# Optimization experiments

Hardware: AMD Instinct MI355X
Metric: run time of the kernel (lower is better)

The kernel has to match this reference:

```python
import jax, jax.numpy as jnp
import numpy as np

HIDDEN = 1024
HEADS = 16
HEAD_DIM = HIDDEN // HEADS
SCALE = HEAD_DIM ** -0.5


def setup_inputs() -> dict:
    key = jax.random.key(0)
    ks = jax.random.split(key, 7)
    B, N, T = 4, 64, 128
    x = jax.random.normal(ks[0], (B * N, T, HIDDEN), dtype=jnp.float32)
    bvecs = jax.random.normal(ks[1], (B, T, 3), dtype=jnp.float32)
    w_std = HIDDEN ** -0.5
    qkv_w = jax.random.normal(ks[2], (HIDDEN, 3 * HIDDEN), dtype=jnp.float32) * w_std
    qkv_b = jnp.zeros((3 * HIDDEN,), dtype=jnp.float32)
    proj_w = jax.random.normal(ks[3], (HIDDEN, HIDDEN), dtype=jnp.float32) * w_std
    proj_b = jnp.zeros((HIDDEN,), dtype=jnp.float32)
    angular_bias_scale = jnp.ones((1,), dtype=jnp.float32)
    return {"x": x, "bvecs": bvecs, "qkv_w": qkv_w, "qkv_b": qkv_b,
            "proj_w": proj_w, "proj_b": proj_b,
            "angular_bias_scale": angular_bias_scale}


def reference(x, bvecs, qkv_w, qkv_b, proj_w, proj_b, angular_bias_scale):
    BN, T, D = x.shape
    B = bvecs.shape[0]
    N = BN // B
    # QKV projection -> (3, BN, H, T, hd)
    qkv = (x @ qkv_w + qkv_b).reshape(BN, T, 3, HEADS, HEAD_DIM)
    qkv = jnp.transpose(qkv, (2, 0, 3, 1, 4))
    q, k, v = qkv[0], qkv[1], qkv[2]
    # normalize b-vectors and compute per-batch angular cosine similarity (B, T, T)
    bvecs_n = bvecs / (jnp.linalg.norm(bvecs, axis=-1, keepdims=True) + 1e-6)
    cos_sim = jnp.clip(jnp.einsum('bid,bjd->bij', bvecs_n, bvecs_n), -1.0, 1.0)
    # repeat across the N patches per batch -> (BN, 1, T, T)
    angular_bias = jnp.repeat(cos_sim, N, axis=0)[:, None, :, :]
    attn_logits = jnp.einsum('bhid,bhjd->bhij', q, k) * SCALE
    attn = jax.nn.softmax(attn_logits + angular_bias_scale * angular_bias, axis=-1)
    out = jnp.einsum('bhij,bhjd->bhid', attn, v)
    out = jnp.transpose(out, (0, 2, 1, 3)).reshape(BN, T, D)
    return out @ proj_w + proj_b
```

## Files before the change

### kernel.cpp

```cpp
#include <hip/hip_runtime.h>
#include <hip/hip_bf16.h>
#include <stdint.h>


typedef float f32x4 __attribute__((ext_vector_type(4)));
typedef __bf16 bf16x8 __attribute__((ext_vector_type(8)));
typedef unsigned short us8 __attribute__((ext_vector_type(8)));
typedef unsigned short u16;

#define MROWS 32768

static __device__ __forceinline__ u16 bfbits(float f) {
  __bf16 h = (__bf16)f;
  return __builtin_bit_cast(u16, h);
}
static __device__ __forceinline__ float bff(u16 u) {
  return (float)__builtin_bit_cast(__bf16, u);
}
static __device__ __forceinline__ void gld16(const void* g, void* l) {
  __builtin_amdgcn_global_load_lds(
      (const __attribute__((address_space(1))) void*)g,
      (__attribute__((address_space(3))) void*)l, 16, 0, 0);
}
static __device__ __forceinline__ f32x4 mfma16(bf16x8 a, bf16x8 b, f32x4 c) {
  return __builtin_amdgcn_mfma_f32_16x16x32_bf16(a, b, c, 0, 0, 0);
}

__global__ __launch_bounds__(256) void k_split(const float* __restrict__ x,
                                               u16* __restrict__ xhl, int n4) {
  int i = blockIdx.x * 256 + threadIdx.x;
  if (i >= n4) return;
  float4 v = ((const float4*)x)[i];
  ushort4 h, l;
  h.x = bfbits(v.x); l.x = bfbits(v.x - bff(h.x));
  h.y = bfbits(v.y); l.y = bfbits(v.y - bff(h.y));
  h.z = bfbits(v.z); l.z = bfbits(v.z - bff(h.z));
  h.w = bfbits(v.w); l.w = bfbits(v.w - bff(h.w));
  int i4 = i << 2;
  int r = i4 >> 10, k = i4 & 1023;
  size_t o = ((size_t)r << 11) + (size_t)((k >> 5) << 6) + (k & 31);
  *(ushort4*)(xhl + o) = h;
  *(ushort4*)(xhl + o + 32) = l;
}

__global__ void k_tsplit(const float* __restrict__ w, u16* __restrict__ thl,
                         int K, int N, int remap) {
  __shared__ float tile[32][33];
  int n0 = blockIdx.x * 32, k0 = blockIdx.y * 32;
  int tx = threadIdx.x, ty = threadIdx.y;
#pragma unroll
  for (int j = 0; j < 32; j += 8)
    tile[ty + j][tx] = w[(size_t)(k0 + ty + j) * N + n0 + tx];
  __syncthreads();
#pragma unroll
  for (int j = 0; j < 32; j += 8) {
    float v = tile[tx][ty + j];
    int n = n0 + ty + j;
    int orow = n;
    if (remap) {
      int s = n >> 10, hid = n & 1023;
      orow = (hid >> 8) * 768 + s * 256 + (hid & 255);
    }
    int k = k0 + tx;
    size_t o = ((size_t)orow << 11) + (size_t)((k >> 5) << 6) + (k & 31);
    u16 hb = bfbits(v);
    thl[o] = hb;
    thl[o + 32] = bfbits(v - bff(hb));
  }
}

__global__ void k_gbias(const float* __restrict__ b, float* __restrict__ gb) {
  int n = blockIdx.x * 256 + threadIdx.x;
  if (n >= 3072) return;
  int s = n >> 10, hid = n & 1023;
  gb[(hid >> 8) * 768 + s * 256 + (hid & 255)] = b[n];
}

__global__ void k_cos(const float* __restrict__ bv, float* __restrict__ cosb) {
  int b = blockIdx.x, t = threadIdx.x;
  __shared__ float nb[128][3];
  float x = bv[(b * 128 + t) * 3 + 0];
  float y = bv[(b * 128 + t) * 3 + 1];
  float z = bv[(b * 128 + t) * 3 + 2];
  float inv = 1.0f / (sqrtf(x * x + y * y + z * z) + 1e-6f);
  nb[t][0] = x * inv; nb[t][1] = y * inv; nb[t][2] = z * inv;
  __syncthreads();
  float xn = nb[t][0], yn = nb[t][1], zn = nb[t][2];
  for (int j = 0; j < 128; j++) {
    float c = xn * nb[j][0] + yn * nb[j][1] + zn * nb[j][2];
    c = fminf(1.0f, fmaxf(-1.0f, c));
    cosb[((size_t)b * 128 + t) * 128 + j] = c;
  }
}

template <int AMODE, int MODE>
__global__ __launch_bounds__(512, 2) void k_gemm(
    const u16* __restrict__ Ahl, const float* __restrict__ Af,
    const u16* __restrict__ Bhl, const float* __restrict__ bias,
    float* __restrict__ C) {
  __shared__ __align__(16) u16 sA[3][128 * 64];
  __shared__ __align__(16) u16 sB[3][256 * 64];
  int tid = threadIdx.x;
  int wave = tid >> 6, lane = tid & 63;
  int fr = lane & 15, fq = lane >> 4;
  int wm = wave >> 2, wn = wave & 3;

  int nT = gridDim.y;
  int h = blockIdx.y * gridDim.x + blockIdx.x;
  int nwg = gridDim.x * gridDim.y;
  int w = (h & 7) * (nwg >> 3) + (h >> 3);
  int rowBase = (w / nT) * 128, colBase = (w % nT) * 256;

  f32x4 acc[4][4];
#pragma unroll
  for (int i = 0; i < 4; i++)
#pragma unroll
    for (int j = 0; j < 4; j++) acc[i][j] = (f32x4){0.f, 0.f, 0.f, 0.f};

  int lr = lane >> 3, ls = (lane & 7) ^ lr;
  const u16* aS = Ahl + (size_t)(rowBase + lr) * 2048 + ls * 8;
  const u16* bS = Bhl + (size_t)(colBase + lr) * 2048 + ls * 8;

  auto stageB = [&](int t, int buf) {
#pragma unroll
    for (int q = 0; q < 4; q++) {
      int R = (q * 8 + wave) * 8;
      gld16(bS + (size_t)R * 2048 + t * 64, &sB[buf][R * 64]);
    }
  };
  auto stageA0 = [&](int t, int buf) {
#pragma unroll
    for (int q = 0; q < 2; q++) {
      int R = (q * 8 + wave) * 8;
      gld16(aS + (size_t)R * 2048 + t * 64, &sA[buf][R * 64]);
    }
  };
  auto stageA1 = [&](int t, int buf) {
    int row = tid >> 2, cs = tid & 3;
    const float* src = Af + (size_t)(rowBase + row) * 1024 + t * 32 + cs * 8;
    float4 v0 = *(const float4*)src;
    float4 v1 = *(const float4*)(src + 4);
    float vv[8] = {v0.x, v0.y, v0.z, v0.w, v1.x, v1.y, v1.z, v1.w};
    us8 hv, lv;
#pragma unroll
    for (int i = 0; i < 8; i++) {
      u16 hb = bfbits(vv[i]);
      hv[i] = hb;
      lv[i] = bfbits(vv[i] - bff(hb));
    }
    int sw = row & 7;
    *(us8*)(&sA[buf][row * 64 + ((cs ^ sw) << 3)]) = hv;
    *(us8*)(&sA[buf][row * 64 + (((cs + 4) ^ sw) << 3)]) = lv;
  };
  auto stage = [&](int t, int buf) {
    stageB(t, buf);
    if constexpr (AMODE == 0) stageA0(t, buf);
    else stageA1(t, buf);
  };

  auto tile = [&](int t, int cur, int nbuf, int vmode) {
    const u16* lA = &sA[cur][0];
    const u16* lB = &sB[cur][0];
    bf16x8 fbh[4], fbl[4];
#pragma unroll
    for (int ni = 0; ni < 4; ni++) {
      int c = wn * 64 + ni * 16 + fr;
      int sw = c & 7;
      fbh[ni] = *(const bf16x8*)(&lB[c * 64 + ((fq ^ sw) << 3)]);
      fbl[ni] = *(const bf16x8*)(&lB[c * 64 + (((fq + 4) ^ sw) << 3)]);
    }
    if (t + 2 < 32) stage(t + 2, nbuf);
#pragma unroll
    for (int mi = 0; mi < 4; mi++) {
      bf16x8 fah, fal;
      int r = wm * 64 + mi * 16 + fr;
      int sw = r & 7;
      fah = *(const bf16x8*)(&lA[r * 64 + ((fq ^ sw) << 3)]);
      fal = *(const bf16x8*)(&lA[r * 64 + (((fq + 4) ^ sw) << 3)]);
#pragma unroll
      for (int ni = 0; ni < 4; ni++) {
        acc[mi][ni] = mfma16(fah, fbh[ni], acc[mi][ni]);
        acc[mi][ni] = mfma16(fah, fbl[ni], acc[mi][ni]);
        acc[mi][ni] = mfma16(fal, fbh[ni], acc[mi][ni]);
      }
    }
    if constexpr (AMODE == 1) {
      if (vmode >= 0)
        asm volatile("s_waitcnt vmcnt(0) lgkmcnt(0)" ::: "memory");
    } else {
      if (vmode == 6)
        asm volatile("s_waitcnt vmcnt(6)" ::: "memory");
      else if (vmode == 0)
        asm volatile("s_waitcnt vmcnt(0)" ::: "memory");
    }
    __builtin_amdgcn_s_barrier();
  };

  stage(0, 0);
  stage(1, 1);
  if constexpr (AMODE == 0) {
    asm volatile("s_waitcnt vmcnt(6)" ::: "memory");
  } else {
    asm volatile("s_waitcnt vmcnt(0) lgkmcnt(0)" ::: "memory");
  }
  __builtin_amdgcn_s_barrier();

#pragma unroll 1
  for (int tb = 0; tb < 30; tb += 3) {
    tile(tb, 0, 2, 6);
    tile(tb + 1, 1, 0, 6);
    tile(tb + 2, 2, 1, 6);
  }
  tile(30, 0, 2, 0);
  tile(31, 1, 0, -1);

  u16* C16 = (u16*)C;
#pragma unroll
  for (int mi = 0; mi < 4; mi++)
#pragma unroll
    for (int ni = 0; ni < 4; ni++)
#pragma unroll
      for (int rr = 0; rr < 4; rr++) {
        int row = rowBase + wm * 64 + mi * 16 + fq * 4 + rr;
        int col = colBase + wn * 64 + ni * 16 + fr;
        float v = acc[mi][ni][rr] + bias[col];
        if constexpr (MODE == 0) {
          int s = col >> 8, hl2 = (col >> 6) & 3, d = col & 63;
          int bn = row >> 7, t = row & 127;
          size_t tb_ = (size_t)(bn * 4 + hl2) * 16384;
          u16 hb = bfbits(v);
          u16 lb = bfbits(v - bff(hb));
          size_t o;
          if (s == 2) {
            o = (size_t)33554432 + tb_ + (size_t)((t >> 6) << 12) + d * 64 +
                ((((t >> 3) & 7) ^ (d & 7)) << 3) + (t & 7);
          } else {
            o = (size_t)s * 16777216 + tb_ + t * 64 +
                (((d >> 3) ^ (t & 7)) << 3) + (d & 7);
          }
          C16[o] = hb;
          C16[o + 8192] = lb;
        } else {
          C[(size_t)row * 1024 + col] = v;
        }
      }
}

__global__ __launch_bounds__(256) void k_attn(
    const u16* __restrict__ Qp, const u16* __restrict__ Kp,
    const u16* __restrict__ Vp, const float* __restrict__ cosb,
    const float* __restrict__ absSp, u16* __restrict__ Ohl, int g) {
  __shared__ __align__(16) u16 sKV[2][2][4096];
  __shared__ __align__(16) float sS[64 * 132];
  u16* sP = (u16*)sS;

  int bx = blockIdx.x;
  int half = bx & 1, hl = (bx >> 1) & 3, bn = bx >> 3, b = bn >> 6;
  int tid = threadIdx.x, wave = tid >> 6, lane = tid & 63;
  int fr = lane & 15, fq = lane >> 4;
  size_t tbase = (size_t)(bn * 4 + hl) * 16384;
  float absS = absSp[0];

  const u16* Qt = Qp + tbase;
  const u16* Kt = Kp + tbase;
  const u16* Vt = Vp + tbase;

  auto stageK = [&](int kt, int buf) {
#pragma unroll
    for (int p2 = 0; p2 < 2; p2++)
#pragma unroll
      for (int q = 0; q < 2; q++) {
        int seg = (q * 4 + wave) * 512;
        gld16(Kt + p2 * 8192 + kt * 4096 + seg + lane * 8, &sKV[buf][p2][seg]);
      }
  };
  auto stageV = [&](int vt, int buf) {
#pragma unroll
    for (int p2 = 0; p2 < 2; p2++)
#pragma unroll
      for (int q = 0; q < 2; q++) {
        int seg = (q * 4 + wave) * 512;
        gld16(Vt + p2 * 8192 + vt * 4096 + seg + lane * 8, &sKV[buf][p2][seg]);
      }
  };

  stageK(0, 0);
  __builtin_amdgcn_sched_barrier(0);
  int rowl = wave * 16 + fr;
  int tq = half * 64 + rowl;
  bf16x8 qh[2], ql[2];
#pragma unroll
  for (int ki = 0; ki < 2; ki++) {
    int sl = ((ki * 4 + fq) ^ (tq & 7)) << 3;
    qh[ki] = *(const bf16x8*)(Qt + tq * 64 + sl);
    ql[ki] = *(const bf16x8*)(Qt + 8192 + tq * 64 + sl);
  }
  __builtin_amdgcn_sched_barrier(0);
  stageK(1, 1);
  __builtin_amdgcn_sched_barrier(0);
  asm volatile("s_waitcnt vmcnt(4)" ::: "memory");
  __builtin_amdgcn_s_barrier();

#pragma unroll
  for (int kt = 0; kt < 2; kt++) {
#pragma unroll
    for (int nt = 0; nt < 4; nt++) {
      f32x4 a = (f32x4){0.f, 0.f, 0.f, 0.f};
      int cl = nt * 16 + fr;
#pragma unroll
      for (int ki = 0; ki < 2; ki++) {
        int sl = ((ki * 4 + fq) ^ (cl & 7)) << 3;
        bf16x8 kh = *(const bf16x8*)(&sKV[kt][0][cl * 64 + sl]);
        bf16x8 kl = *(const bf16x8*)(&sKV[kt][1][cl * 64 + sl]);
        a = mfma16(qh[ki], kh, a);
        a = mfma16(qh[ki], kl, a);
        a = mfma16(ql[ki], kh, a);
      }
#pragma unroll
      for (int rr = 0; rr < 4; rr++) {
        int rl = wave * 16 + fq * 4 + rr;
        int col = kt * 64 + nt * 16 + fr;
        int tg = half * 64 + rl;
        float cv = cosb[((size_t)(b * 128 + tg)) * 128 + col];
        sS[rl * 132 + col] = a[rr] * 0.125f + absS * cv;
      }
    }
    __builtin_amdgcn_s_barrier();
    if (kt == 0) {
      stageV(0, 0);
      __builtin_amdgcn_sched_barrier(0);
      asm volatile("s_waitcnt vmcnt(4)" ::: "memory");
      __builtin_amdgcn_s_barrier();
    }
  }
  stageV(1, 1);
  __builtin_amdgcn_sched_barrier(0);

  for (int r = 0; r < 16; r++) {
    int tl = wave * 16 + r;
    float s0 = sS[tl * 132 + lane], s1 = sS[tl * 132 + 64 + lane];
    float m = fmaxf(s0, s1);
#pragma unroll
    for (int off = 32; off >= 1; off >>= 1) m = fmaxf(m, __shfl_xor(m, off));
    float p0 = __expf(s0 - m), p1 = __expf(s1 - m);
    float sum = p0 + p1;
#pragma unroll
    for (int off = 32; off >= 1; off >>= 1) sum += __shfl_xor(sum, off);
    float inv = 1.0f / sum;
    p0 *= inv; p1 *= inv;
    u16 h0 = bfbits(p0), h1 = bfbits(p1);
    sP[tl * 264 + lane] = h0;
    sP[tl * 264 + 64 + lane] = h1;
    sP[tl * 264 + 128 + lane] = bfbits(p0 - bff(h0));
    sP[tl * 264 + 192 + lane] = bfbits(p1 - bff(h1));
  }

  f32x4 accO[4];
#pragma unroll
  for (int nt = 0; nt < 4; nt++) accO[nt] = (f32x4){0.f, 0.f, 0.f, 0.f};
#pragma unroll
  for (int vt = 0; vt < 2; vt++) {
    if (vt == 0) {
      asm volatile("s_waitcnt vmcnt(4)" ::: "memory");
    } else {
      asm volatile("s_waitcnt vmcnt(0)" ::: "memory");
    }
    __builtin_amdgcn_s_barrier();
    bf16x8 ph[2], pl[2];
#pragma unroll
    for (int ki = 0; ki < 2; ki++) {
      ph[ki] = *(const bf16x8*)(&sP[rowl * 264 + vt * 64 + ki * 32 + fq * 8]);
      pl[ki] = *(const bf16x8*)(&sP[rowl * 264 + 128 + vt * 64 + ki * 32 + fq * 8]);
    }
#pragma unroll
    for (int nt = 0; nt < 4; nt++) {
      int d = nt * 16 + fr;
#pragma unroll
      for (int ki = 0; ki < 2; ki++) {
        int sl = ((ki * 4 + fq) ^ (d & 7)) << 3;
        bf16x8 vh = *(const bf16x8*)(&sKV[vt][0][d * 64 + sl]);
        bf16x8 vl = *(const bf16x8*)(&sKV[vt][1][d * 64 + sl]);
        accO[nt] = mfma16(ph[ki], vh, accO[nt]);
        accO[nt] = mfma16(ph[ki], vl, accO[nt]);
        accO[nt] = mfma16(pl[ki], vh, accO[nt]);
      }
    }
  }

  int hg = g * 4 + hl;
#pragma unroll
  for (int nt = 0; nt < 4; nt++)
#pragma unroll
    for (int rr = 0; rr < 4; rr++) {
      int tl = wave * 16 + fq * 4 + rr;
      int tg = half * 64 + tl;
      int d = nt * 16 + fr;
      float v = accO[nt][rr];
      size_t o = ((size_t)(bn * 128 + tg) << 11) +
                 (size_t)(hg * 2 + (d >> 5)) * 64 + (d & 31);
      u16 hh = bfbits(v);
      Ohl[o] = hh;
      Ohl[o + 32] = bfbits(v - bff(hh));
    }
}

extern "C" void kernel_launch(void* const* d_in, const int* in_sizes, int n_in,
                              void* d_out, int out_size, void* d_ws,
                              size_t ws_size, hipStream_t stream) {
  const float* x = (const float*)d_in[0];
  const float* bv = (const float*)d_in[1];
  const float* qkvw = (const float*)d_in[2];
  const float* qkvb = (const float*)d_in[3];
  const float* projw = (const float*)d_in[4];
  const float* projb = (const float*)d_in[5];
  const float* absS = (const float*)d_in[6];
  float* out = (float*)d_out;

  char* ws = (char*)d_ws;
  size_t off = 0;
  auto alloc = [&](size_t b) {
    char* p = ws + off;
    off += (b + 255) & ~(size_t)255;
    return p;
  };
  u16* wqhl = (u16*)alloc((size_t)3072 * 2048 * 2);
  u16* wphl = (u16*)alloc((size_t)1024 * 2048 * 2);
  float* gbias = (float*)alloc(3072 * 4);
  float* cosb = (float*)alloc((size_t)4 * 128 * 128 * 4);
  u16* Ohl = (u16*)alloc((size_t)MROWS * 2048 * 2);
  u16* xhl = (u16*)alloc((size_t)MROWS * 2048 * 2);
  bool planA = (off <= ws_size);

  u16* O16 = (u16*)d_out;

  k_tsplit<<<dim3(96, 32), dim3(32, 8), 0, stream>>>(qkvw, wqhl, 1024, 3072, 1);
  k_tsplit<<<dim3(32, 32), dim3(32, 8), 0, stream>>>(projw, wphl, 1024, 1024, 0);
  k_gbias<<<dim3(12), dim3(256), 0, stream>>>(qkvb, gbias);
  k_cos<<<dim3(4), dim3(128), 0, stream>>>(bv, cosb);
  if (planA)
    k_split<<<dim3(32768), dim3(256), 0, stream>>>(x, xhl, 8388608);

  for (int g = 0; g < 4; g++) {
    const u16* bw = wqhl + (size_t)g * 768 * 2048;
    if (planA)
      k_gemm<0, 0><<<dim3(256, 3), dim3(512), 0, stream>>>(
          xhl, nullptr, bw, gbias + g * 768, (float*)O16);
    else
      k_gemm<1, 0><<<dim3(256, 3), dim3(512), 0, stream>>>(
          nullptr, x, bw, gbias + g * 768, (float*)O16);
    k_attn<<<dim3(2048), dim3(256), 0, stream>>>(
        O16, O16 + 16777216, O16 + 33554432, cosb, absS, Ohl, g);
  }

  k_gemm<0, 1><<<dim3(256, 4), dim3(512), 0, stream>>>(
      Ohl, nullptr, wphl, projb, out);
}
```

Measured before the change: 1.299 ms.

## Stage GEMM and attention epilogues through LDS for coalesced 16-byte stores

The QKV GEMM epilogue now writes its hi/lo bf16 split outputs into a shared-memory tile, then copies the whole contiguous block to global memory with 16-byte vector stores instead of scattered 2-byte stores. The attention kernel likewise stages its output in LDS before writing coalesced uint4 rows. The attention block index is remapped so blocks are grouped differently across dispatch, and s_setprio raises wave priority around the MFMA loops. This trades extra barriers and LDS traffic for far fewer, wider global writes.

Measured after the change: 1.198 ms. -7.8%, faster.

```diff
diff --git a/kernel.cpp b/kernel.cpp
--- a/kernel.cpp
+++ b/kernel.cpp
@@ -98,8 +98,9 @@
     const u16* __restrict__ Ahl, const float* __restrict__ Af,
     const u16* __restrict__ Bhl, const float* __restrict__ bias,
     float* __restrict__ C) {
-  __shared__ __align__(16) u16 sA[3][128 * 64];
-  __shared__ __align__(16) u16 sB[3][256 * 64];
+  __shared__ __align__(16) u16 smem[73728];
+  u16* sAb = smem;
+  u16* sBb = smem + 24576;
   int tid = threadIdx.x;
   int wave = tid >> 6, lane = tid & 63;
   int fr = lane & 15, fq = lane >> 4;
@@ -125,14 +126,14 @@
 #pragma unroll
     for (int q = 0; q < 4; q++) {
       int R = (q * 8 + wave) * 8;
-      gld16(bS + (size_t)R * 2048 + t * 64, &sB[buf][R * 64]);
+      gld16(bS + (size_t)R * 2048 + t * 64, &sBb[buf * 16384 + R * 64]);
     }
   };
   auto stageA0 = [&](int t, int buf) {
 #pragma unroll
     for (int q = 0; q < 2; q++) {
       int R = (q * 8 + wave) * 8;
-      gld16(aS + (size_t)R * 2048 + t * 64, &sA[buf][R * 64]);
+      gld16(aS + (size_t)R * 2048 + t * 64, &sAb[buf * 8192 + R * 64]);
     }
   };
   auto stageA1 = [&](int t, int buf) {
@@ -149,8 +150,8 @@
       lv[i] = bfbits(vv[i] - bff(hb));
     }
     int sw = row & 7;
-    *(us8*)(&sA[buf][row * 64 + ((cs ^ sw) << 3)]) = hv;
-    *(us8*)(&sA[buf][row * 64 + (((cs + 4) ^ sw) << 3)]) = lv;
+    *(us8*)(&sAb[buf * 8192 + row * 64 + ((cs ^ sw) << 3)]) = hv;
+    *(us8*)(&sAb[buf * 8192 + row * 64 + (((cs + 4) ^ sw) << 3)]) = lv;
   };
   auto stage = [&](int t, int buf) {
     stageB(t, buf);
@@ -159,8 +160,8 @@
   };
 
   auto tile = [&](int t, int cur, int nbuf, int vmode) {
-    const u16* lA = &sA[cur][0];
-    const u16* lB = &sB[cur][0];
+    const u16* lA = &sAb[cur * 8192];
+    const u16* lB = &sBb[cur * 16384];
     bf16x8 fbh[4], fbl[4];
 #pragma unroll
     for (int ni = 0; ni < 4; ni++) {
@@ -214,36 +215,49 @@
   tile(30, 0, 2, 0);
   tile(31, 1, 0, -1);
 
-  u16* C16 = (u16*)C;
-#pragma unroll
-  for (int mi = 0; mi < 4; mi++)
-#pragma unroll
-    for (int ni = 0; ni < 4; ni++)
-#pragma unroll
-      for (int rr = 0; rr < 4; rr++) {
-        int row = rowBase + wm * 64 + mi * 16 + fq * 4 + rr;
-        int col = colBase + wn * 64 + ni * 16 + fr;
-        float v = acc[mi][ni][rr] + bias[col];
-        if constexpr (MODE == 0) {
-          int s = col >> 8, hl2 = (col >> 6) & 3, d = col & 63;
-          int bn = row >> 7, t = row & 127;
-          size_t tb_ = (size_t)(bn * 4 + hl2) * 16384;
+  if constexpr (MODE == 0) {
+    int s = colBase >> 8;
+    int bn = rowBase >> 7;
+#pragma unroll
+    for (int mi = 0; mi < 4; mi++)
+#pragma unroll
+      for (int ni = 0; ni < 4; ni++)
+#pragma unroll
+        for (int rr = 0; rr < 4; rr++) {
+          int t = wm * 64 + mi * 16 + fq * 4 + rr;
+          int c256 = wn * 64 + ni * 16 + fr;
+          int d = c256 & 63;
+          float v = acc[mi][ni][rr] + bias[colBase + c256];
           u16 hb = bfbits(v);
           u16 lb = bfbits(v - bff(hb));
-          size_t o;
-          if (s == 2) {
-            o = (size_t)33554432 + tb_ + (size_t)((t >> 6) << 12) + d * 64 +
-                ((((t >> 3) & 7) ^ (d & 7)) << 3) + (t & 7);
-          } else {
-            o = (size_t)s * 16777216 + tb_ + t * 64 +
-                (((d >> 3) ^ (t & 7)) << 3) + (d & 7);
-          }
-          C16[o] = hb;
-          C16[o + 8192] = lb;
-        } else {
-          C[(size_t)row * 1024 + col] = v;
+          int loff;
+          if (s == 2)
+            loff = wn * 16384 + ((t >> 6) << 12) + d * 64 +
+                   ((((t >> 3) & 7) ^ (d & 7)) << 3) + (t & 7);
+          else
+            loff = wn * 16384 + t * 64 + (((d >> 3) ^ (t & 7)) << 3) + (d & 7);
+          smem[loff] = hb;
+          smem[loff + 8192] = lb;
         }
-      }
+    __syncthreads();
+    u16* C16 = (u16*)C;
+    size_t gbase = (size_t)s * 16777216 + (size_t)bn * 65536;
+    const uint4* srcv = (const uint4*)smem;
+    uint4* dstv = (uint4*)(C16 + gbase);
+#pragma unroll
+    for (int i = 0; i < 16; i++) dstv[i * 512 + tid] = srcv[i * 512 + tid];
+  } else {
+#pragma unroll
+    for (int mi = 0; mi < 4; mi++)
+#pragma unroll
+      for (int ni = 0; ni < 4; ni++)
+#pragma unroll
+        for (int rr = 0; rr < 4; rr++) {
+          int row = rowBase + wm * 64 + mi * 16 + fq * 4 + rr;
+          int col = colBase + wn * 64 + ni * 16 + fr;
+          C[(size_t)row * 1024 + col] = acc[mi][ni][rr] + bias[col];
+        }
+  }
 }
 
 __global__ __launch_bounds__(256) void k_attn(
@@ -253,9 +267,12 @@
   __shared__ __align__(16) u16 sKV[2][2][4096];
   __shared__ __align__(16) float sS[64 * 132];
   u16* sP = (u16*)sS;
-
-  int bx = blockIdx.x;
-  int half = bx & 1, hl = (bx >> 1) & 3, bn = bx >> 3, b = bn >> 6;
+  u16* sO = (u16*)sS;
+
+  int v_ = blockIdx.x;
+  int pair = (v_ & 7) * 128 + ((v_ >> 3) >> 1);
+  int half = (v_ >> 3) & 1;
+  int hl = pair & 3, bn = pair >> 2, b = bn >> 6;
   int tid = threadIdx.x, wave = tid >> 6, lane = tid & 63;
   int fr = lane & 15, fq = lane >> 4;
   size_t tbase = (size_t)(bn * 4 + hl) * 16384;
@@ -303,6 +320,7 @@
 
 #pragma unroll
   for (int kt = 0; kt < 2; kt++) {
+    __builtin_amdgcn_s_setprio(1);
 #pragma unroll
     for (int nt = 0; nt < 4; nt++) {
       f32x4 a = (f32x4){0.f, 0.f, 0.f, 0.f};
@@ -325,6 +343,7 @@
         sS[rl * 132 + col] = a[rr] * 0.125f + absS * cv;
       }
     }
+    __builtin_amdgcn_s_setprio(0);
     __builtin_amdgcn_s_barrier();
     if (kt == 0) {
       stageV(0, 0);
@@ -372,6 +391,7 @@
       ph[ki] = *(const bf16x8*)(&sP[rowl * 264 + vt * 64 + ki * 32 + fq * 8]);
       pl[ki] = *(const bf16x8*)(&sP[rowl * 264 + 128 + vt * 64 + ki * 32 + fq * 8]);
     }
+    __builtin_amdgcn_s_setprio(1);
 #pragma unroll
     for (int nt = 0; nt < 4; nt++) {
       int d = nt * 16 + fr;
@@ -385,23 +405,33 @@
         accO[nt] = mfma16(pl[ki], vh, accO[nt]);
       }
     }
-  }
-
-  int hg = g * 4 + hl;
+    __builtin_amdgcn_s_setprio(0);
+  }
+
+  __syncthreads();
 #pragma unroll
   for (int nt = 0; nt < 4; nt++)
 #pragma unroll
     for (int rr = 0; rr < 4; rr++) {
       int tl = wave * 16 + fq * 4 + rr;
-      int tg = half * 64 + tl;
       int d = nt * 16 + fr;
       float v = accO[nt][rr];
-      size_t o = ((size_t)(bn * 128 + tg) << 11) +
-                 (size_t)(hg * 2 + (d >> 5)) * 64 + (d & 31);
       u16 hh = bfbits(v);
-      Ohl[o] = hh;
-      Ohl[o + 32] = bfbits(v - bff(hh));
-    }
+      u16 ll = bfbits(v - bff(hh));
+      int off = tl * 136 + ((d >> 5) << 6) + (d & 31);
+      sO[off] = hh;
+      sO[off + 32] = ll;
+    }
+  __syncthreads();
+  int hg = g * 4 + hl;
+#pragma unroll
+  for (int i = 0; i < 4; i++) {
+    int c = i * 256 + tid;
+    int r = c >> 4, w16 = (c & 15) << 3;
+    uint4 val = *(const uint4*)(&sO[r * 136 + w16]);
+    size_t go = ((size_t)(bn * 128 + half * 64 + r) << 11) + hg * 128 + w16;
+    *(uint4*)(Ohl + go) = val;
+  }
 }
 
 extern "C" void kernel_launch(void* const* d_in, const int* in_sizes, int n_in,
```
